# Optimization experiments

Hardware: AMD Instinct MI355X
Metric: run time of the kernel (lower is better)

The kernel has to match this reference:

```python
import jax, jax.numpy as jnp
import numpy as np

B, N, E = 16, 64, 512
C_IMG = 512
H1, H2, H3 = 256, 128, 64
U, R = 8, 8
BBC = 9
EH1, EH2 = 64, 64
BBOX_POS_MAX = 1024.0
EPS = 1e-5


def setup_inputs():
    key = jax.random.key(0)
    ks = jax.random.split(key, 24)
    f = lambda i, shape, s=0.05: jax.random.normal(ks[i], shape, jnp.float32) * s
    return {
        'roi_features': f(0, (B, N, C_IMG), 1.0),
        'batch_bboxes': jax.random.uniform(ks[1], (B, N, 4)) * BBOX_POS_MAX,
        'batch_directions': jax.random.uniform(ks[2], (B, N, 4)),
        'batch_priorities': jax.random.uniform(ks[3], (B, N)),
        'w1': f(4, (C_IMG, H1)), 'b1': f(5, (H1,)),
        'bn1_g': jnp.ones((H1,)), 'bn1_b': jnp.zeros((H1,)),
        'bn1_m': jnp.zeros((H1,)), 'bn1_v': jnp.ones((H1,)),
        'w2': f(6, (H1, H2)), 'b2': f(7, (H2,)),
        'bn2_g': jnp.ones((H2,)), 'bn2_b': jnp.zeros((H2,)),
        'bn2_m': jnp.zeros((H2,)), 'bn2_v': jnp.ones((H2,)),
        'w3': f(8, (H2, H3)), 'b3': f(9, (H3,)),
        'wn': f(10, (H3, U)), 'bn_c': f(11, (U,)),
        'we1': f(12, (2 * BBC, EH1)), 'be1': f(13, (EH1,)),
        'we2': f(14, (EH1, EH2)), 'be2': f(15, (EH2,)),
        'wei': f(16, (EH2, R)), 'bei': f(17, (R,)),
        'edge_index': jax.random.randint(ks[18], (B, 2, E), 0, N, dtype=jnp.int32),
    }


def _bn(x, g, b, m, v):
    # BatchNorm1d in eval mode (running stats)
    return (x - m) * jax.lax.rsqrt(v + EPS) * g + b


def _build_see(edge_index):
    # Padded neighbor table replacing edge_index2dict:
    # see[b,n,0] = n, then srcs of edges with dst==n, in original edge order.
    src = edge_index[:, 0, :]                                   # [B,E]
    dst = edge_index[:, 1, :]                                   # [B,E]
    eq = dst[:, :, None] == dst[:, None, :]                     # [B,E,E]
    lower = jnp.tril(jnp.ones((E, E), bool), -1)
    pos = jnp.sum(eq & lower, axis=-1) + 1                      # rank within dst group, +1 for self slot
    see = jnp.zeros((B, N, N), jnp.int32).at[:, :, 0].set(jnp.arange(N, dtype=jnp.int32))
    b_idx = jnp.arange(B)[:, None]
    see = see.at[b_idx, dst, pos].set(src, mode='drop')
    deg = jnp.zeros((B, N), jnp.int32).at[b_idx, dst].add(1)
    count = jnp.minimum(deg + 1, N)
    mask = (jnp.arange(N)[None, None, :] < count[:, :, None]).astype(jnp.float32)  # [B,N,N]
    return see, mask


def _forward(roi_features, batch_bboxes, batch_directions, batch_priorities,
             w1, b1, bn1_g, bn1_b, bn1_m, bn1_v,
             w2, b2, bn2_g, bn2_b, bn2_m, bn2_v,
             w3, b3, wn, bn_c,
             we1, be1, we2, be2, wei, bei, edge_index):
    see, mask = _build_see(edge_index)
    # --- node branch (node_predictor + node_concept_interpreter) ---
    x = roi_features.reshape(B * N, C_IMG)
    x = jax.nn.relu(_bn(x @ w1 + b1, bn1_g, bn1_b, bn1_m, bn1_v))
    x = jax.nn.relu(_bn(x @ w2 + b2, bn2_g, bn2_b, bn2_m, bn2_v))
    x = jax.nn.relu(x @ w3 + b3)
    node_c = jax.nn.sigmoid(x @ wn + bn_c).reshape(B, N, U)
    # get_nlm_unary_concepts: gather per-node neighborhood into dense [B,N,N,U]
    gu = jax.vmap(lambda u, s: u[s])(node_c, see)               # [B,N,N,U]
    node_concepts = (gu * mask[..., None]).reshape(B * N, N, U)
    # --- edge branch ---
    attr = jnp.concatenate([batch_bboxes / BBOX_POS_MAX, batch_directions,
                            batch_priorities[..., None]], axis=-1)  # [B,N,BBC]
    pair = jnp.concatenate([
        jnp.broadcast_to(attr[:, :, None, :], (B, N, N, BBC)),
        jnp.broadcast_to(attr[:, None, :, :], (B, N, N, BBC))], axis=-1).reshape(-1, 2 * BBC)
    e = jax.nn.relu(pair @ we1 + be1)
    e = jax.nn.relu(e @ we2 + be2)
    rel = jax.nn.sigmoid(e @ wei + bei).reshape(B, N, N, R)
    # get_nlm_binary_concepts: rel[b, see[b,n,i], see[b,n,j]] with zero padding
    def per_b(r, s, m):
        g = r[s[:, :, None], s[:, None, :]]                     # [N,N,N,R]
        return g * (m[:, :, None, None] * m[:, None, :, None])
    edge_concepts = jax.vmap(per_b)(rel, see, mask).reshape(B * N, N, N, R)
    return node_concepts, edge_concepts


def reference(roi_features, batch_bboxes, batch_directions, batch_priorities,
              w1, b1, bn1_g, bn1_b, bn1_m, bn1_v,
              w2, b2, bn2_g, bn2_b, bn2_m, bn2_v,
              w3, b3, wn, bn_c,
              we1, be1, we2, be2, wei, bei, edge_index):
    return _forward(roi_features, batch_bboxes, batch_directions, batch_priorities,
                    w1, b1, bn1_g, bn1_b, bn1_m, bn1_v,
                    w2, b2, bn2_g, bn2_b, bn2_m, bn2_v,
                    w3, b3, wn, bn_c,
                    we1, be1, we2, be2, wei, bei, edge_index)
```

## Files before the change

### kernel.cpp

```cpp
#include <hip/hip_runtime.h>
#include <math.h>

#define BB    16
#define NN    64
#define EE    512
#define CIMG  512
#define H1D   256
#define H2D   128
#define H3D   64
#define UD    8
#define RD    8
#define BBCD  9
#define EH1D  64
#define EH2D  64
#define EPSF  1e-5f

typedef float nfloat4 __attribute__((ext_vector_type(4)));

__global__ __launch_bounds__(256) void fusedA_kernel(
    const int* __restrict__ edge_index,
    const float* __restrict__ bboxes,
    const float* __restrict__ dirs,
    const float* __restrict__ prios,
    const float* __restrict__ we1, const float* __restrict__ be1,
    int* __restrict__ see, int* __restrict__ cnt,
    const float* __restrict__ roi,
    const float* __restrict__ w1, const float* __restrict__ b1,
    const float* __restrict__ g1, const float* __restrict__ bt1,
    const float* __restrict__ m1, const float* __restrict__ v1,
    const float* __restrict__ w2, const float* __restrict__ b2,
    const float* __restrict__ g2, const float* __restrict__ bt2,
    const float* __restrict__ m2, const float* __restrict__ v2,
    const float* __restrict__ w3, const float* __restrict__ b3,
    const float* __restrict__ wn, const float* __restrict__ bnc,
    float* __restrict__ node_c,
    const float* __restrict__ we2, const float* __restrict__ be2,
    const float* __restrict__ wei, const float* __restrict__ bei,
    float* __restrict__ rel)
{
    __shared__ union {
        struct {
            int src[EE];
            int dst[EE];
            int see[NN * NN];
        } p;
        struct {
            float part[4096];
            float h1[4][H1D];
            float h2[4][H2D];
            float h3[4][H3D];
        } n;
        struct {
            float e1[NN * 68];
            float qw[NN * EH1D];
            float wei[EH2D * RD];
            float attr[NN][BBCD];
            float we1[2 * BBCD * EH1D];
            float Pi[EH1D];
            float be2[EH2D];
            float bei[RD];
        } e;
    } sm;

    const int t = threadIdx.x;

    if (blockIdx.x < BB) {
        const int b = blockIdx.x;
        const int* ei = edge_index + b * 2 * EE;
        for (int e = t; e < EE; e += 256) {
            sm.p.src[e] = ei[e];
            sm.p.dst[e] = ei[EE + e];
        }
        for (int x = t; x < NN * NN; x += 256)
            sm.p.see[x] = ((x & (NN - 1)) == 0) ? (x >> 6) : 0;
        __syncthreads();

        if (t < NN) {
            int pos = 0;
            #pragma unroll 8
            for (int e = 0; e < EE; ++e) {
                if (sm.p.dst[e] == t) {
                    ++pos;
                    if (pos < NN) sm.p.see[t * NN + pos] = sm.p.src[e];
                }
            }
            int c = pos + 1;
            cnt[b * NN + t] = (c < NN) ? c : NN;
        }
        __syncthreads();

        int4* dst4 = (int4*)(see + b * NN * NN);
        const int4* src4 = (const int4*)sm.p.see;
        for (int x = t; x < (NN * NN) / 4; x += 256) dst4[x] = src4[x];
        return;
    }

    if (blockIdx.x >= BB + 256) {
        const int id = blockIdx.x - (BB + 256);
        const int b = id >> 6;
        const int i = id & 63;

        if (t < NN) {
            const float* bbp = bboxes + (b * NN + t) * 4;
            const float* ddp = dirs + (b * NN + t) * 4;
            sm.e.attr[t][0] = bbp[0] * (1.0f / 1024.0f);
            sm.e.attr[t][1] = bbp[1] * (1.0f / 1024.0f);
            sm.e.attr[t][2] = bbp[2] * (1.0f / 1024.0f);
            sm.e.attr[t][3] = bbp[3] * (1.0f / 1024.0f);
            sm.e.attr[t][4] = ddp[0];
            sm.e.attr[t][5] = ddp[1];
            sm.e.attr[t][6] = ddp[2];
            sm.e.attr[t][7] = ddp[3];
            sm.e.attr[t][8] = prios[b * NN + t];
        }
        for (int x = t; x < 2 * BBCD * EH1D; x += 256) sm.e.we1[x] = we1[x];
        {
            const float4* w4 = (const float4*)we2;
            float4* qw4 = (float4*)sm.e.qw;
            #pragma unroll
            for (int x = 0; x < 4; ++x) qw4[x * 256 + t] = w4[x * 256 + t];
        }
        if (t < 128) ((float4*)sm.e.wei)[t] = ((const float4*)wei)[t];
        if (t < EH2D) sm.e.be2[t] = be2[t];
        if (t < RD) sm.e.bei[t] = bei[t];
        __syncthreads();

        if (t < EH1D) {
            float p = be1[t];
            #pragma unroll
            for (int c = 0; c < BBCD; ++c)
                p = fmaf(sm.e.attr[i][c], sm.e.we1[c * EH1D + t], p);
            sm.e.Pi[t] = p;
        }
        __syncthreads();

        {
            const int o = t & 63;
            const int jw = t >> 6;
            #pragma unroll
            for (int jg = 0; jg < 16; ++jg) {
                const int j = jg * 4 + jw;
                float a = sm.e.Pi[o];
                #pragma unroll
                for (int c = 0; c < BBCD; ++c)
                    a = fmaf(sm.e.attr[j][c], sm.e.we1[(BBCD + c) * EH1D + o], a);
                sm.e.e1[j * 68 + o] = fmaxf(0.f, a);
            }
        }
        __syncthreads();

        const int tx = t & 15, ty = t >> 4;
        const int o0 = tx * 4, j0 = ty * 4;
        float acc[4][4];
        #pragma unroll
        for (int r = 0; r < 4; ++r)
            #pragma unroll
            for (int o = 0; o < 4; ++o) acc[r][o] = 0.f;

        #pragma unroll 4
        for (int cg = 0; cg < 16; ++cg) {
            float ev[4][4];
            #pragma unroll
            for (int r = 0; r < 4; ++r) {
                float4 v = *(const float4*)(sm.e.e1 + (j0 + r) * 68 + cg * 4);
                ev[r][0] = v.x; ev[r][1] = v.y; ev[r][2] = v.z; ev[r][3] = v.w;
            }
            #pragma unroll
            for (int q = 0; q < 4; ++q) {
                float4 wv = *(const float4*)(sm.e.qw + (cg * 4 + q) * EH1D + o0);
                #pragma unroll
                for (int r = 0; r < 4; ++r) {
                    acc[r][0] = fmaf(ev[r][q], wv.x, acc[r][0]);
                    acc[r][1] = fmaf(ev[r][q], wv.y, acc[r][1]);
                    acc[r][2] = fmaf(ev[r][q], wv.z, acc[r][2]);
                    acc[r][3] = fmaf(ev[r][q], wv.w, acc[r][3]);
                }
            }
        }

        {
            float4 bv = *(const float4*)(sm.e.be2 + o0);
            #pragma unroll
            for (int r = 0; r < 4; ++r) {
                float4 v;
                v.x = fmaxf(0.f, acc[r][0] + bv.x);
                v.y = fmaxf(0.f, acc[r][1] + bv.y);
                v.z = fmaxf(0.f, acc[r][2] + bv.z);
                v.w = fmaxf(0.f, acc[r][3] + bv.w);
                *(float4*)(sm.e.e1 + (j0 + r) * 68 + o0) = v;
            }
        }
        __syncthreads();

        {
            const int j = t >> 2;
            const int r0 = (t & 3) * 2;
            float a0 = sm.e.bei[r0], a1 = sm.e.bei[r0 + 1];
            const float* e2row = sm.e.e1 + j * 68;
            #pragma unroll
            for (int og = 0; og < 16; ++og) {
                float4 e2v = *(const float4*)(e2row + og * 4);
                float2 w0 = *(const float2*)(sm.e.wei + (og * 4 + 0) * RD + r0);
                float2 w1 = *(const float2*)(sm.e.wei + (og * 4 + 1) * RD + r0);
                float2 w2 = *(const float2*)(sm.e.wei + (og * 4 + 2) * RD + r0);
                float2 w3 = *(const float2*)(sm.e.wei + (og * 4 + 3) * RD + r0);
                a0 = fmaf(e2v.x, w0.x, a0); a1 = fmaf(e2v.x, w0.y, a1);
                a0 = fmaf(e2v.y, w1.x, a0); a1 = fmaf(e2v.y, w1.y, a1);
                a0 = fmaf(e2v.z, w2.x, a0); a1 = fmaf(e2v.z, w2.y, a1);
                a0 = fmaf(e2v.w, w3.x, a0); a1 = fmaf(e2v.w, w3.y, a1);
            }
            float2 o;
            o.x = 1.f / (1.f + expf(-a0));
            o.y = 1.f / (1.f + expf(-a1));
            *(float2*)(rel + ((size_t)id * NN + j) * RD + r0) = o;
        }
        return;
    }

    const int row0 = (blockIdx.x - BB) * 4;
    float* part = sm.n.part;

    {
        const int og = t & 63, kg = t >> 6;
        const float4* w1v = (const float4*)w1;
        const float4* roiv = (const float4*)(roi + (size_t)row0 * CIMG);
        float acc[4][4];
        #pragma unroll
        for (int r = 0; r < 4; ++r)
            #pragma unroll
            for (int c = 0; c < 4; ++c) acc[r][c] = 0.f;

        for (int cq = 0; cq < 32; ++cq) {
            const int c4 = kg * 32 + cq;
            float x[4][4], w[4][4];
            #pragma unroll
            for (int r = 0; r < 4; ++r) {
                float4 v = roiv[r * 128 + c4];
                x[r][0] = v.x; x[r][1] = v.y; x[r][2] = v.z; x[r][3] = v.w;
            }
            #pragma unroll
            for (int q = 0; q < 4; ++q) {
                float4 v = w1v[(size_t)(c4 * 4 + q) * 64 + og];
                w[q][0] = v.x; w[q][1] = v.y; w[q][2] = v.z; w[q][3] = v.w;
            }
            #pragma unroll
            for (int r = 0; r < 4; ++r)
                #pragma unroll
                for (int q = 0; q < 4; ++q)
                    #pragma unroll
                    for (int c = 0; c < 4; ++c)
                        acc[r][c] = fmaf(x[r][q], w[q][c], acc[r][c]);
        }
        #pragma unroll
        for (int r = 0; r < 4; ++r) {
            float4 v = {acc[r][0], acc[r][1], acc[r][2], acc[r][3]};
            *(float4*)(part + (kg * 4 + r) * 256 + og * 4) = v;
        }
    }
    __syncthreads();
    {
        const int o = t;
        const float bias = b1[o];
        const float scale = rsqrtf(v1[o] + EPSF) * g1[o];
        const float beta = bt1[o];
        const float mu = m1[o];
        #pragma unroll
        for (int r = 0; r < 4; ++r) {
            float s = part[(0 * 4 + r) * 256 + o] + part[(1 * 4 + r) * 256 + o]
                    + part[(2 * 4 + r) * 256 + o] + part[(3 * 4 + r) * 256 + o];
            sm.n.h1[r][o] = fmaxf(0.f, (s + bias - mu) * scale + beta);
        }
    }
    __syncthreads();

    {
        const int og = t & 31, kg = t >> 5;
        const float4* w2v = (const float4*)w2;
        float acc[4][4];
        #pragma unroll
        for (int r = 0; r < 4; ++r)
            #pragma unroll
            for (int c = 0; c < 4; ++c) acc[r][c] = 0.f;

        #pragma unroll
        for (int cq = 0; cq < 8; ++cq) {
            const int c4 = kg * 8 + cq;
            float x[4][4], w[4][4];
            #pragma unroll
            for (int r = 0; r < 4; ++r) {
                float4 v = *(const float4*)&sm.n.h1[r][c4 * 4];
                x[r][0] = v.x; x[r][1] = v.y; x[r][2] = v.z; x[r][3] = v.w;
            }
            #pragma unroll
            for (int q = 0; q < 4; ++q) {
                float4 v = w2v[(size_t)(c4 * 4 + q) * 32 + og];
                w[q][0] = v.x; w[q][1] = v.y; w[q][2] = v.z; w[q][3] = v.w;
            }
            #pragma unroll
            for (int r = 0; r < 4; ++r)
                #pragma unroll
                for (int q = 0; q < 4; ++q)
                    #pragma unroll
                    for (int c = 0; c < 4; ++c)
                        acc[r][c] = fmaf(x[r][q], w[q][c], acc[r][c]);
        }
        #pragma unroll
        for (int r = 0; r < 4; ++r) {
            float4 v = {acc[r][0], acc[r][1], acc[r][2], acc[r][3]};
            *(float4*)(part + (kg * 4 + r) * 128 + og * 4) = v;
        }
    }
    __syncthreads();
    {
        const int o = t & 127;
        const int rp = t >> 7;
        const float bias = b2[o];
        const float scale = rsqrtf(v2[o] + EPSF) * g2[o];
        const float beta = bt2[o];
        const float mu = m2[o];
        #pragma unroll
        for (int rr = 0; rr < 2; ++rr) {
            const int r = rp + rr * 2;
            float s = 0.f;
            #pragma unroll
            for (int kg = 0; kg < 8; ++kg) s += part[(kg * 4 + r) * 128 + o];
            sm.n.h2[r][o] = fmaxf(0.f, (s + bias - mu) * scale + beta);
        }
    }
    __syncthreads();

    {
        const int og = t & 15, kg = t >> 4;
        const float4* w3v = (const float4*)w3;
        float acc[4][4];
        #pragma unroll
        for (int r = 0; r < 4; ++r)
            #pragma unroll
            for (int c = 0; c < 4; ++c) acc[r][c] = 0.f;

        #pragma unroll
        for (int cq = 0; cq < 2; ++cq) {
            const int c4 = kg * 2 + cq;
            float x[4][4], w[4][4];
            #pragma unroll
            for (int r = 0; r < 4; ++r) {
                float4 v = *(const float4*)&sm.n.h2[r][c4 * 4];
                x[r][0] = v.x; x[r][1] = v.y; x[r][2] = v.z; x[r][3] = v.w;
            }
            #pragma unroll
            for (int q = 0; q < 4; ++q) {
                float4 v = w3v[(size_t)(c4 * 4 + q) * 16 + og];
                w[q][0] = v.x; w[q][1] = v.y; w[q][2] = v.z; w[q][3] = v.w;
            }
            #pragma unroll
            for (int r = 0; r < 4; ++r)
                #pragma unroll
                for (int q = 0; q < 4; ++q)
                    #pragma unroll
                    for (int c = 0; c < 4; ++c)
                        acc[r][c] = fmaf(x[r][q], w[q][c], acc[r][c]);
        }
        #pragma unroll
        for (int r = 0; r < 4; ++r) {
            float4 v = {acc[r][0], acc[r][1], acc[r][2], acc[r][3]};
            *(float4*)(part + (kg * 4 + r) * 64 + og * 4) = v;
        }
    }
    __syncthreads();
    {
        const int o = t & 63;
        const int r = t >> 6;
        float s = b3[o];
        #pragma unroll
        for (int kg = 0; kg < 16; ++kg) s += part[(kg * 4 + r) * 64 + o];
        sm.n.h3[r][o] = fmaxf(0.f, s);
    }
    __syncthreads();

    if (t < 32) {
        const int o = t & 7, r = t >> 3;
        float a = bnc[o];
        #pragma unroll 8
        for (int c = 0; c < H3D; ++c) a = fmaf(sm.n.h3[r][c], wn[c * UD + o], a);
        node_c[(size_t)(row0 + r) * UD + o] = 1.f / (1.f + expf(-a));
    }
}

__global__ __launch_bounds__(256) void gatherfill_kernel(
    const int* __restrict__ see, const int* __restrict__ cnt,
    const float* __restrict__ node_c, const float* __restrict__ rel,
    float* __restrict__ out_node, float* __restrict__ out_edge)
{
    __shared__ int s_s[NN];

    const int t = threadIdx.x;
    const int bi = blockIdx.x;
    const int b = bi >> 6;
    const int c = cnt[bi];

    if (t < NN) s_s[t] = see[bi * NN + t];
    __syncthreads();

    if (t < NN) {
        const float m = (t < c) ? 1.f : 0.f;
        const float4* src = (const float4*)(node_c + (size_t)(b * NN + s_s[t]) * UD);
        float4 v0 = src[0], v1 = src[1];
        v0.x *= m; v0.y *= m; v0.z *= m; v0.w *= m;
        v1.x *= m; v1.y *= m; v1.z *= m; v1.w *= m;
        float4* dst = (float4*)(out_node + ((size_t)bi * NN + t) * UD);
        dst[0] = v0;
        dst[1] = v1;
    }

    const float* relb = rel + (size_t)b * NN * NN * RD;
    float* outb = out_edge + (size_t)bi * NN * NN * RD;
    const nfloat4 z = {0.f, 0.f, 0.f, 0.f};

    #pragma unroll
    for (int it = 0; it < (NN * NN) / 256; ++it) {
        const int task = it * 256 + t;
        const int j = task >> 6;
        const int k = task & 63;
        nfloat4* dst = (nfloat4*)(outb + (size_t)task * RD);
        if (j < c) {
            if (k < c) {
                const float4* src =
                    (const float4*)(relb + (size_t)(s_s[j] * NN + s_s[k]) * RD);
                float4 v0 = src[0], v1 = src[1];
                ((float4*)dst)[0] = v0;
                ((float4*)dst)[1] = v1;
            } else {
                __builtin_nontemporal_store(z, dst);
                __builtin_nontemporal_store(z, dst + 1);
            }
        } else {
            __builtin_nontemporal_store(z, dst);
            __builtin_nontemporal_store(z, dst + 1);
        }
    }
}

extern "C" void kernel_launch(void* const* d_in, const int* in_sizes, int n_in,
                              void* d_out, int out_size, void* d_ws, size_t ws_size,
                              hipStream_t stream)
{
    const float* roi  = (const float*)d_in[0];
    const float* bbox = (const float*)d_in[1];
    const float* dirs = (const float*)d_in[2];
    const float* prio = (const float*)d_in[3];
    const float* w1   = (const float*)d_in[4];
    const float* b1   = (const float*)d_in[5];
    const float* g1   = (const float*)d_in[6];
    const float* bt1  = (const float*)d_in[7];
    const float* m1   = (const float*)d_in[8];
    const float* v1   = (const float*)d_in[9];
    const float* w2   = (const float*)d_in[10];
    const float* b2   = (const float*)d_in[11];
    const float* g2   = (const float*)d_in[12];
    const float* bt2  = (const float*)d_in[13];
    const float* m2   = (const float*)d_in[14];
    const float* v2   = (const float*)d_in[15];
    const float* w3   = (const float*)d_in[16];
    const float* b3   = (const float*)d_in[17];
    const float* wn   = (const float*)d_in[18];
    const float* bnc  = (const float*)d_in[19];
    const float* we1  = (const float*)d_in[20];
    const float* be1  = (const float*)d_in[21];
    const float* we2  = (const float*)d_in[22];
    const float* be2  = (const float*)d_in[23];
    const float* wei  = (const float*)d_in[24];
    const float* bei  = (const float*)d_in[25];
    const int* edge_index = (const int*)d_in[26];

    char* ws = (char*)d_ws;
    int*   see    = (int*)ws;   ws += (size_t)BB * NN * NN * 4;
    int*   cnt    = (int*)ws;   ws += (size_t)BB * NN * 4;
    float* node_c = (float*)ws; ws += (size_t)BB * NN * UD * 4;
    float* rel    = (float*)ws; ws += (size_t)BB * NN * NN * RD * 4;

    float* out_node = (float*)d_out;
    float* out_edge = (float*)d_out + (size_t)BB * NN * NN * UD;

    hipLaunchKernelGGL(fusedA_kernel,
                       dim3(BB + 256 + BB * NN), dim3(256), 0, stream,
                       edge_index, bbox, dirs, prio, we1, be1,
                       see, cnt,
                       roi, w1, b1, g1, bt1, m1, v1,
                       w2, b2, g2, bt2, m2, v2,
                       w3, b3, wn, bnc, node_c,
                       we2, be2, wei, bei, rel);
    hipLaunchKernelGGL(gatherfill_kernel, dim3(BB * NN), dim3(256), 0, stream,
                       see, cnt, node_c, rel, out_node, out_edge);
}
```

Before: 246.6 us.

## Move edge output zero-fill into first kernel and copy only valid corner

Adds extra blocks to the fused first kernel that zero the entire edge-concept output with nontemporal stores, so the fill overlaps with node and edge MLP compute. The second kernel now writes only the valid c-by-c corner gathered from rel, with no branching per element. Separately, the row mapping in the edge MLP tile is changed to interleave rows, to alter the LDS access pattern. Corner elements are written twice, which relies on ordering across kernels on the same stream.

```diff
diff --git a/kernel.cpp b/kernel.cpp
--- a/kernel.cpp
+++ b/kernel.cpp
@@ -16,6 +16,12 @@
 #define EPSF  1e-5f
 
 typedef float nfloat4 __attribute__((ext_vector_type(4)));
+
+#define GRID_PREP  BB
+#define GRID_NODE  256
+#define GRID_EDGE  (BB * NN)
+#define GRID_FILL  2048
+#define FILL_BASE  (GRID_PREP + GRID_NODE + GRID_EDGE)
 
 __global__ __launch_bounds__(256) void fusedA_kernel(
     const int* __restrict__ edge_index,
@@ -36,8 +42,21 @@
     float* __restrict__ node_c,
     const float* __restrict__ we2, const float* __restrict__ be2,
     const float* __restrict__ wei, const float* __restrict__ bei,
-    float* __restrict__ rel)
+    float* __restrict__ rel,
+    float* __restrict__ out_edge)
 {
+    const int t = threadIdx.x;
+
+    if (blockIdx.x >= FILL_BASE) {
+        const int f = blockIdx.x - FILL_BASE;
+        const nfloat4 z = {0.f, 0.f, 0.f, 0.f};
+        float* base = out_edge + (size_t)f * 16384 + t * 4;
+        #pragma unroll
+        for (int i = 0; i < 16; ++i)
+            __builtin_nontemporal_store(z, (nfloat4*)(base + i * 1024));
+        return;
+    }
+
     __shared__ union {
         struct {
             int src[EE];
@@ -62,8 +81,6 @@
         } e;
     } sm;
 
-    const int t = threadIdx.x;
-
     if (blockIdx.x < BB) {
         const int b = blockIdx.x;
         const int* ei = edge_index + b * 2 * EE;
@@ -95,8 +112,8 @@
         return;
     }
 
-    if (blockIdx.x >= BB + 256) {
-        const int id = blockIdx.x - (BB + 256);
+    if (blockIdx.x >= BB + GRID_NODE) {
+        const int id = blockIdx.x - (BB + GRID_NODE);
         const int b = id >> 6;
         const int i = id & 63;
 
@@ -150,7 +167,7 @@
         __syncthreads();
 
         const int tx = t & 15, ty = t >> 4;
-        const int o0 = tx * 4, j0 = ty * 4;
+        const int o0 = tx * 4;
         float acc[4][4];
         #pragma unroll
         for (int r = 0; r < 4; ++r)
@@ -162,7 +179,7 @@
             float ev[4][4];
             #pragma unroll
             for (int r = 0; r < 4; ++r) {
-                float4 v = *(const float4*)(sm.e.e1 + (j0 + r) * 68 + cg * 4);
+                float4 v = *(const float4*)(sm.e.e1 + (ty + 16 * r) * 68 + cg * 4);
                 ev[r][0] = v.x; ev[r][1] = v.y; ev[r][2] = v.z; ev[r][3] = v.w;
             }
             #pragma unroll
@@ -187,7 +204,7 @@
                 v.y = fmaxf(0.f, acc[r][1] + bv.y);
                 v.z = fmaxf(0.f, acc[r][2] + bv.z);
                 v.w = fmaxf(0.f, acc[r][3] + bv.w);
-                *(float4*)(sm.e.e1 + (j0 + r) * 68 + o0) = v;
+                *(float4*)(sm.e.e1 + (ty + 16 * r) * 68 + o0) = v;
             }
         }
         __syncthreads();
@@ -386,7 +403,7 @@
     }
 }
 
-__global__ __launch_bounds__(256) void gatherfill_kernel(
+__global__ __launch_bounds__(256) void corner_kernel(
     const int* __restrict__ see, const int* __restrict__ cnt,
     const float* __restrict__ node_c, const float* __restrict__ rel,
     float* __restrict__ out_node, float* __restrict__ out_edge)
@@ -414,28 +431,18 @@
 
     const float* relb = rel + (size_t)b * NN * NN * RD;
     float* outb = out_edge + (size_t)bi * NN * NN * RD;
-    const nfloat4 z = {0.f, 0.f, 0.f, 0.f};
-
-    #pragma unroll
-    for (int it = 0; it < (NN * NN) / 256; ++it) {
-        const int task = it * 256 + t;
-        const int j = task >> 6;
-        const int k = task & 63;
-        nfloat4* dst = (nfloat4*)(outb + (size_t)task * RD);
-        if (j < c) {
-            if (k < c) {
-                const float4* src =
-                    (const float4*)(relb + (size_t)(s_s[j] * NN + s_s[k]) * RD);
-                float4 v0 = src[0], v1 = src[1];
-                ((float4*)dst)[0] = v0;
-                ((float4*)dst)[1] = v1;
-            } else {
-                __builtin_nontemporal_store(z, dst);
-                __builtin_nontemporal_store(z, dst + 1);
-            }
-        } else {
-            __builtin_nontemporal_store(z, dst);
-            __builtin_nontemporal_store(z, dst + 1);
+
+    const int w = t >> 6;
+    const int k = t & 63;
+    if (k < c) {
+        const int sk = s_s[k];
+        for (int j = w; j < c; j += 4) {
+            const float4* src =
+                (const float4*)(relb + (size_t)(s_s[j] * NN + sk) * RD);
+            float4 v0 = src[0], v1 = src[1];
+            float4* dst = (float4*)(outb + (size_t)(j * NN + k) * RD);
+            dst[0] = v0;
+            dst[1] = v1;
         }
     }
 }
@@ -482,13 +489,14 @@
     float* out_edge = (float*)d_out + (size_t)BB * NN * NN * UD;
 
     hipLaunchKernelGGL(fusedA_kernel,
-                       dim3(BB + 256 + BB * NN), dim3(256), 0, stream,
+                       dim3(FILL_BASE + GRID_FILL), dim3(256), 0, stream,
                        edge_index, bbox, dirs, prio, we1, be1,
                        see, cnt,
                        roi, w1, b1, g1, bt1, m1, v1,
                        w2, b2, g2, bt2, m2, v2,
                        w3, b3, wn, bnc, node_c,
-                       we2, be2, wei, bei, rel);
-    hipLaunchKernelGGL(gatherfill_kernel, dim3(BB * NN), dim3(256), 0, stream,
+                       we2, be2, wei, bei, rel,
+                       out_edge);
+    hipLaunchKernelGGL(corner_kernel, dim3(BB * NN), dim3(256), 0, stream,
                        see, cnt, node_c, rel, out_node, out_edge);
 }
```

New measurement: 234.7 us. 1.05x faster.

## Recompute edge MLP per output slab and drop rel workspace gather

Applied to the files above, without the earlier changes.

The edge MLP no longer runs once per (b,i) row into a global rel buffer that a second kernel gathers from. The edge-slab kernel now evaluates the MLP only for the c×c valid (j,k) pairs of each slab, using precomputed per-neighbor P/Q projections, and writes sigmoid outputs straight into the output. Padded regions get nontemporal zero stores. This removes the rel workspace write and its gathered re-read, at the cost of duplicated MLP work across slabs that share a batch and an extra per-tile synchronization loop.

```diff
diff --git a/kernel.cpp b/kernel.cpp
--- a/kernel.cpp
+++ b/kernel.cpp
@@ -17,12 +17,9 @@
 
 typedef float nfloat4 __attribute__((ext_vector_type(4)));
 
-__global__ __launch_bounds__(256) void fusedA_kernel(
+
+__global__ __launch_bounds__(256) void prepnode_kernel(
     const int* __restrict__ edge_index,
-    const float* __restrict__ bboxes,
-    const float* __restrict__ dirs,
-    const float* __restrict__ prios,
-    const float* __restrict__ we1, const float* __restrict__ be1,
     int* __restrict__ see, int* __restrict__ cnt,
     const float* __restrict__ roi,
     const float* __restrict__ w1, const float* __restrict__ b1,
@@ -33,10 +30,7 @@
     const float* __restrict__ m2, const float* __restrict__ v2,
     const float* __restrict__ w3, const float* __restrict__ b3,
     const float* __restrict__ wn, const float* __restrict__ bnc,
-    float* __restrict__ node_c,
-    const float* __restrict__ we2, const float* __restrict__ be2,
-    const float* __restrict__ wei, const float* __restrict__ bei,
-    float* __restrict__ rel)
+    float* __restrict__ node_c)
 {
     __shared__ union {
         struct {
@@ -50,16 +44,6 @@
             float h2[4][H2D];
             float h3[4][H3D];
         } n;
-        struct {
-            float e1[NN * 68];
-            float qw[NN * EH1D];
-            float wei[EH2D * RD];
-            float attr[NN][BBCD];
-            float we1[2 * BBCD * EH1D];
-            float Pi[EH1D];
-            float be2[EH2D];
-            float bei[RD];
-        } e;
     } sm;
 
     const int t = threadIdx.x;
@@ -95,91 +79,334 @@
         return;
     }
 
-    if (blockIdx.x >= BB + 256) {
-        const int id = blockIdx.x - (BB + 256);
-        const int b = id >> 6;
-        const int i = id & 63;
-
-        if (t < NN) {
-            const float* bbp = bboxes + (b * NN + t) * 4;
-            const float* ddp = dirs + (b * NN + t) * 4;
-            sm.e.attr[t][0] = bbp[0] * (1.0f / 1024.0f);
-            sm.e.attr[t][1] = bbp[1] * (1.0f / 1024.0f);
-            sm.e.attr[t][2] = bbp[2] * (1.0f / 1024.0f);
-            sm.e.attr[t][3] = bbp[3] * (1.0f / 1024.0f);
-            sm.e.attr[t][4] = ddp[0];
-            sm.e.attr[t][5] = ddp[1];
-            sm.e.attr[t][6] = ddp[2];
-            sm.e.attr[t][7] = ddp[3];
-            sm.e.attr[t][8] = prios[b * NN + t];
-        }
-        for (int x = t; x < 2 * BBCD * EH1D; x += 256) sm.e.we1[x] = we1[x];
+    const int row0 = (blockIdx.x - BB) * 4;
+    float* part = sm.n.part;
+
+    {
+        const int og = t & 63, kg = t >> 6;
+        const float4* w1v = (const float4*)w1;
+        const float4* roiv = (const float4*)(roi + (size_t)row0 * CIMG);
+        float acc[4][4];
+        #pragma unroll
+        for (int r = 0; r < 4; ++r)
+            #pragma unroll
+            for (int c = 0; c < 4; ++c) acc[r][c] = 0.f;
+
+        for (int cq = 0; cq < 32; ++cq) {
+            const int c4 = kg * 32 + cq;
+            float x[4][4], w[4][4];
+            #pragma unroll
+            for (int r = 0; r < 4; ++r) {
+                float4 v = roiv[r * 128 + c4];
+                x[r][0] = v.x; x[r][1] = v.y; x[r][2] = v.z; x[r][3] = v.w;
+            }
+            #pragma unroll
+            for (int q = 0; q < 4; ++q) {
+                float4 v = w1v[(size_t)(c4 * 4 + q) * 64 + og];
+                w[q][0] = v.x; w[q][1] = v.y; w[q][2] = v.z; w[q][3] = v.w;
+            }
+            #pragma unroll
+            for (int r = 0; r < 4; ++r)
+                #pragma unroll
+                for (int q = 0; q < 4; ++q)
+                    #pragma unroll
+                    for (int c = 0; c < 4; ++c)
+                        acc[r][c] = fmaf(x[r][q], w[q][c], acc[r][c]);
+        }
+        #pragma unroll
+        for (int r = 0; r < 4; ++r) {
+            float4 v = {acc[r][0], acc[r][1], acc[r][2], acc[r][3]};
+            *(float4*)(part + (kg * 4 + r) * 256 + og * 4) = v;
+        }
+    }
+    __syncthreads();
+    {
+        const int o = t;
+        const float bias = b1[o];
+        const float scale = rsqrtf(v1[o] + EPSF) * g1[o];
+        const float beta = bt1[o];
+        const float mu = m1[o];
+        #pragma unroll
+        for (int r = 0; r < 4; ++r) {
+            float s = part[(0 * 4 + r) * 256 + o] + part[(1 * 4 + r) * 256 + o]
+                    + part[(2 * 4 + r) * 256 + o] + part[(3 * 4 + r) * 256 + o];
+            sm.n.h1[r][o] = fmaxf(0.f, (s + bias - mu) * scale + beta);
+        }
+    }
+    __syncthreads();
+
+    {
+        const int og = t & 31, kg = t >> 5;
+        const float4* w2v = (const float4*)w2;
+        float acc[4][4];
+        #pragma unroll
+        for (int r = 0; r < 4; ++r)
+            #pragma unroll
+            for (int c = 0; c < 4; ++c) acc[r][c] = 0.f;
+
+        #pragma unroll
+        for (int cq = 0; cq < 8; ++cq) {
+            const int c4 = kg * 8 + cq;
+            float x[4][4], w[4][4];
+            #pragma unroll
+            for (int r = 0; r < 4; ++r) {
+                float4 v = *(const float4*)&sm.n.h1[r][c4 * 4];
+                x[r][0] = v.x; x[r][1] = v.y; x[r][2] = v.z; x[r][3] = v.w;
+            }
+            #pragma unroll
+            for (int q = 0; q < 4; ++q) {
+                float4 v = w2v[(size_t)(c4 * 4 + q) * 32 + og];
+                w[q][0] = v.x; w[q][1] = v.y; w[q][2] = v.z; w[q][3] = v.w;
+            }
+            #pragma unroll
+            for (int r = 0; r < 4; ++r)
+                #pragma unroll
+                for (int q = 0; q < 4; ++q)
+                    #pragma unroll
+                    for (int c = 0; c < 4; ++c)
+                        acc[r][c] = fmaf(x[r][q], w[q][c], acc[r][c]);
+        }
+        #pragma unroll
+        for (int r = 0; r < 4; ++r) {
+            float4 v = {acc[r][0], acc[r][1], acc[r][2], acc[r][3]};
+            *(float4*)(part + (kg * 4 + r) * 128 + og * 4) = v;
+        }
+    }
+    __syncthreads();
+    {
+        const int o = t & 127;
+        const int rp = t >> 7;
+        const float bias = b2[o];
+        const float scale = rsqrtf(v2[o] + EPSF) * g2[o];
+        const float beta = bt2[o];
+        const float mu = m2[o];
+        #pragma unroll
+        for (int rr = 0; rr < 2; ++rr) {
+            const int r = rp + rr * 2;
+            float s = 0.f;
+            #pragma unroll
+            for (int kg = 0; kg < 8; ++kg) s += part[(kg * 4 + r) * 128 + o];
+            sm.n.h2[r][o] = fmaxf(0.f, (s + bias - mu) * scale + beta);
+        }
+    }
+    __syncthreads();
+
+    {
+        const int og = t & 15, kg = t >> 4;
+        const float4* w3v = (const float4*)w3;
+        float acc[4][4];
+        #pragma unroll
+        for (int r = 0; r < 4; ++r)
+            #pragma unroll
+            for (int c = 0; c < 4; ++c) acc[r][c] = 0.f;
+
+        #pragma unroll
+        for (int cq = 0; cq < 2; ++cq) {
+            const int c4 = kg * 2 + cq;
+            float x[4][4], w[4][4];
+            #pragma unroll
+            for (int r = 0; r < 4; ++r) {
+                float4 v = *(const float4*)&sm.n.h2[r][c4 * 4];
+                x[r][0] = v.x; x[r][1] = v.y; x[r][2] = v.z; x[r][3] = v.w;
+            }
+            #pragma unroll
+            for (int q = 0; q < 4; ++q) {
+                float4 v = w3v[(size_t)(c4 * 4 + q) * 16 + og];
+                w[q][0] = v.x; w[q][1] = v.y; w[q][2] = v.z; w[q][3] = v.w;
+            }
+            #pragma unroll
+            for (int r = 0; r < 4; ++r)
+                #pragma unroll
+                for (int q = 0; q < 4; ++q)
+                    #pragma unroll
+                    for (int c = 0; c < 4; ++c)
+                        acc[r][c] = fmaf(x[r][q], w[q][c], acc[r][c]);
+        }
+        #pragma unroll
+        for (int r = 0; r < 4; ++r) {
+            float4 v = {acc[r][0], acc[r][1], acc[r][2], acc[r][3]};
+            *(float4*)(part + (kg * 4 + r) * 64 + og * 4) = v;
+        }
+    }
+    __syncthreads();
+    {
+        const int o = t & 63;
+        const int r = t >> 6;
+        float s = b3[o];
+        #pragma unroll
+        for (int kg = 0; kg < 16; ++kg) s += part[(kg * 4 + r) * 64 + o];
+        sm.n.h3[r][o] = fmaxf(0.f, s);
+    }
+    __syncthreads();
+
+    if (t < 32) {
+        const int o = t & 7, r = t >> 3;
+        float a = bnc[o];
+        #pragma unroll 8
+        for (int c = 0; c < H3D; ++c) a = fmaf(sm.n.h3[r][c], wn[c * UD + o], a);
+        node_c[(size_t)(row0 + r) * UD + o] = 1.f / (1.f + expf(-a));
+    }
+}
+
+__global__ __launch_bounds__(256) void edgeslab_kernel(
+    const float* __restrict__ bboxes,
+    const float* __restrict__ dirs,
+    const float* __restrict__ prios,
+    const float* __restrict__ we1, const float* __restrict__ be1,
+    const float* __restrict__ we2, const float* __restrict__ be2,
+    const float* __restrict__ wei, const float* __restrict__ bei,
+    const int* __restrict__ see, const int* __restrict__ cnt,
+    const float* __restrict__ node_c,
+    float* __restrict__ out_node, float* __restrict__ out_edge)
+{
+    __shared__ float e1L[NN * 68];
+    __shared__ float PL[NN * NN];
+    __shared__ float QL[NN * NN];
+    __shared__ float qwL[NN * EH1D];
+    __shared__ float attrL[NN][BBCD];
+    __shared__ float we1L[2 * BBCD * EH1D];
+    __shared__ float weiL[EH2D * RD];
+    __shared__ float be1L[EH1D];
+    __shared__ float be2L[EH2D];
+    __shared__ float beiL[RD];
+    __shared__ int   sLi[NN];
+    __shared__ int   jkL[64];
+
+    const int t = threadIdx.x;
+    const int bi = blockIdx.x;
+    const int b = bi >> 6;
+    const int c = cnt[bi];
+
+    if (t < NN) sLi[t] = see[bi * NN + t];
+    if (t < NN) {
+        const float* bbp = bboxes + (b * NN + t) * 4;
+        const float* ddp = dirs + (b * NN + t) * 4;
+        attrL[t][0] = bbp[0] * (1.0f / 1024.0f);
+        attrL[t][1] = bbp[1] * (1.0f / 1024.0f);
+        attrL[t][2] = bbp[2] * (1.0f / 1024.0f);
+        attrL[t][3] = bbp[3] * (1.0f / 1024.0f);
+        attrL[t][4] = ddp[0];
+        attrL[t][5] = ddp[1];
+        attrL[t][6] = ddp[2];
+        attrL[t][7] = ddp[3];
+        attrL[t][8] = prios[b * NN + t];
+    }
+    for (int x = t; x < 2 * BBCD * EH1D; x += 256) we1L[x] = we1[x];
+    {
+        const float4* w4 = (const float4*)we2;
+        float4* qw4 = (float4*)qwL;
+        #pragma unroll
+        for (int x = 0; x < 4; ++x) qw4[x * 256 + t] = w4[x * 256 + t];
+    }
+    if (t < 128) ((float4*)weiL)[t] = ((const float4*)wei)[t];
+    if (t < EH1D) be1L[t] = be1[t];
+    if (t < EH2D) be2L[t] = be2[t];
+    if (t < RD)   beiL[t] = bei[t];
+    __syncthreads();
+
+    if (t < NN) {
+        const float m = (t < c) ? 1.f : 0.f;
+        const float4* src = (const float4*)(node_c + (size_t)(b * NN + sLi[t]) * UD);
+        float4 v0 = src[0], v1 = src[1];
+        v0.x *= m; v0.y *= m; v0.z *= m; v0.w *= m;
+        v1.x *= m; v1.y *= m; v1.z *= m; v1.w *= m;
+        float4* dst = (float4*)(out_node + ((size_t)bi * NN + t) * UD);
+        dst[0] = v0;
+        dst[1] = v1;
+    }
+
+    {
+        const int o = t & 63, jw = t >> 6;
+        #pragma unroll
+        for (int jg = 0; jg < 16; ++jg) {
+            const int j = jg * 4 + jw;
+            const int n = sLi[j];
+            float p = be1L[o], q = 0.f;
+            #pragma unroll
+            for (int cc = 0; cc < BBCD; ++cc) {
+                p = fmaf(attrL[n][cc], we1L[cc * EH1D + o], p);
+                q = fmaf(attrL[n][cc], we1L[(BBCD + cc) * EH1D + o], q);
+            }
+            PL[j * NN + o] = p;
+            QL[j * NN + o] = q;
+        }
+    }
+
+    float* slab = out_edge + (size_t)bi * (NN * NN * RD);
+    {
+        const nfloat4 z = {0.f, 0.f, 0.f, 0.f};
+        const int nrow4 = (NN - c) * 128;
+        for (int x = t; x < nrow4; x += 256) {
+            const int row = c + (x >> 7);
+            __builtin_nontemporal_store(
+                z, (nfloat4*)(slab + (size_t)row * 512 + (size_t)(x & 127) * 4));
+        }
+        const int w = NN - c;
+        const int ntail = c * w * 2;
+        for (int x = t; x < ntail; x += 256) {
+            const int e = x >> 1, h = x & 1;
+            const int j = e / w;
+            const int k = c + (e - j * w);
+            __builtin_nontemporal_store(
+                z, (nfloat4*)(slab + (size_t)(j * NN + k) * RD + h * 4));
+        }
+    }
+    __syncthreads();
+
+    const int npairs = c * c;
+    const int ntiles = (npairs + 63) >> 6;
+    for (int tt = 0; tt < ntiles; ++tt) {
+        const int base = tt << 6;
+        if (t < 64) {
+            const int p = base + t;
+            int u = 0xFFFF;
+            if (p < npairs) { const int j = p / c; u = (j << 8) | (p - j * c); }
+            jkL[t] = u;
+        }
+        __syncthreads();
+
         {
-            const float4* w4 = (const float4*)we2;
-            float4* qw4 = (float4*)sm.e.qw;
-            #pragma unroll
-            for (int x = 0; x < 4; ++x) qw4[x * 256 + t] = w4[x * 256 + t];
-        }
-        if (t < 128) ((float4*)sm.e.wei)[t] = ((const float4*)wei)[t];
-        if (t < EH2D) sm.e.be2[t] = be2[t];
-        if (t < RD) sm.e.bei[t] = bei[t];
+            const int o = t & 63, pw = t >> 6;
+            #pragma unroll
+            for (int pg = 0; pg < 16; ++pg) {
+                const int row = pg * 4 + pw;
+                const int u = jkL[row];
+                const int jj = (u >> 8) & 63, kk = u & 63;
+                e1L[row * 68 + o] = fmaxf(0.f, PL[jj * NN + o] + QL[kk * NN + o]);
+            }
+        }
         __syncthreads();
 
-        if (t < EH1D) {
-            float p = be1[t];
-            #pragma unroll
-            for (int c = 0; c < BBCD; ++c)
-                p = fmaf(sm.e.attr[i][c], sm.e.we1[c * EH1D + t], p);
-            sm.e.Pi[t] = p;
-        }
-        __syncthreads();
-
         {
-            const int o = t & 63;
-            const int jw = t >> 6;
-            #pragma unroll
-            for (int jg = 0; jg < 16; ++jg) {
-                const int j = jg * 4 + jw;
-                float a = sm.e.Pi[o];
+            const int tx = t & 15, ty = t >> 4;
+            const int o0 = tx * 4;
+            float acc[4][4];
+            #pragma unroll
+            for (int r = 0; r < 4; ++r)
                 #pragma unroll
-                for (int c = 0; c < BBCD; ++c)
-                    a = fmaf(sm.e.attr[j][c], sm.e.we1[(BBCD + c) * EH1D + o], a);
-                sm.e.e1[j * 68 + o] = fmaxf(0.f, a);
-            }
-        }
-        __syncthreads();
-
-        const int tx = t & 15, ty = t >> 4;
-        const int o0 = tx * 4, j0 = ty * 4;
-        float acc[4][4];
-        #pragma unroll
-        for (int r = 0; r < 4; ++r)
-            #pragma unroll
-            for (int o = 0; o < 4; ++o) acc[r][o] = 0.f;
-
-        #pragma unroll 4
-        for (int cg = 0; cg < 16; ++cg) {
-            float ev[4][4];
-            #pragma unroll
-            for (int r = 0; r < 4; ++r) {
-                float4 v = *(const float4*)(sm.e.e1 + (j0 + r) * 68 + cg * 4);
-                ev[r][0] = v.x; ev[r][1] = v.y; ev[r][2] = v.z; ev[r][3] = v.w;
-            }
-            #pragma unroll
-            for (int q = 0; q < 4; ++q) {
-                float4 wv = *(const float4*)(sm.e.qw + (cg * 4 + q) * EH1D + o0);
+                for (int o = 0; o < 4; ++o) acc[r][o] = 0.f;
+
+            #pragma unroll 4
+            for (int cg = 0; cg < 16; ++cg) {
+                float ev[4][4];
                 #pragma unroll
                 for (int r = 0; r < 4; ++r) {
-                    acc[r][0] = fmaf(ev[r][q], wv.x, acc[r][0]);
-                    acc[r][1] = fmaf(ev[r][q], wv.y, acc[r][1]);
-                    acc[r][2] = fmaf(ev[r][q], wv.z, acc[r][2]);
-                    acc[r][3] = fmaf(ev[r][q], wv.w, acc[r][3]);
+                    float4 v = *(const float4*)(e1L + (ty + 16 * r) * 68 + cg * 4);
+                    ev[r][0] = v.x; ev[r][1] = v.y; ev[r][2] = v.z; ev[r][3] = v.w;
                 }
-            }
-        }
-
-        {
-            float4 bv = *(const float4*)(sm.e.be2 + o0);
+                #pragma unroll
+                for (int q = 0; q < 4; ++q) {
+                    float4 wv = *(const float4*)(qwL + (cg * 4 + q) * EH1D + o0);
+                    #pragma unroll
+                    for (int r = 0; r < 4; ++r) {
+                        acc[r][0] = fmaf(ev[r][q], wv.x, acc[r][0]);
+                        acc[r][1] = fmaf(ev[r][q], wv.y, acc[r][1]);
+                        acc[r][2] = fmaf(ev[r][q], wv.z, acc[r][2]);
+                        acc[r][3] = fmaf(ev[r][q], wv.w, acc[r][3]);
+                    }
+                }
+            }
+            float4 bv = *(const float4*)(be2L + o0);
             #pragma unroll
             for (int r = 0; r < 4; ++r) {
                 float4 v;
@@ -187,256 +414,38 @@
                 v.y = fmaxf(0.f, acc[r][1] + bv.y);
                 v.z = fmaxf(0.f, acc[r][2] + bv.z);
                 v.w = fmaxf(0.f, acc[r][3] + bv.w);
-                *(float4*)(sm.e.e1 + (j0 + r) * 68 + o0) = v;
+                *(float4*)(e1L + (ty + 16 * r) * 68 + o0) = v;
             }
         }
         __syncthreads();
 
         {
-            const int j = t >> 2;
+            const int row = t >> 2;
             const int r0 = (t & 3) * 2;
-            float a0 = sm.e.bei[r0], a1 = sm.e.bei[r0 + 1];
-            const float* e2row = sm.e.e1 + j * 68;
+            const int u = jkL[row];
+            float a0 = beiL[r0], a1 = beiL[r0 + 1];
+            const float* e2row = e1L + row * 68;
             #pragma unroll
             for (int og = 0; og < 16; ++og) {
                 float4 e2v = *(const float4*)(e2row + og * 4);
-                float2 w0 = *(const float2*)(sm.e.wei + (og * 4 + 0) * RD + r0);
-                float2 w1 = *(const float2*)(sm.e.wei + (og * 4 + 1) * RD + r0);
-                float2 w2 = *(const float2*)(sm.e.wei + (og * 4 + 2) * RD + r0);
-                float2 w3 = *(const float2*)(sm.e.wei + (og * 4 + 3) * RD + r0);
+                float2 w0 = *(const float2*)(weiL + (og * 4 + 0) * RD + r0);
+                float2 w1 = *(const float2*)(weiL + (og * 4 + 1) * RD + r0);
+                float2 w2 = *(const float2*)(weiL + (og * 4 + 2) * RD + r0);
+                float2 w3 = *(const float2*)(weiL + (og * 4 + 3) * RD + r0);
                 a0 = fmaf(e2v.x, w0.x, a0); a1 = fmaf(e2v.x, w0.y, a1);
                 a0 = fmaf(e2v.y, w1.x, a0); a1 = fmaf(e2v.y, w1.y, a1);
                 a0 = fmaf(e2v.z, w2.x, a0); a1 = fmaf(e2v.z, w2.y, a1);
                 a0 = fmaf(e2v.w, w3.x, a0); a1 = fmaf(e2v.w, w3.y, a1);
             }
-            float2 o;
-            o.x = 1.f / (1.f + expf(-a0));
-            o.y = 1.f / (1.f + expf(-a1));
-            *(float2*)(rel + ((size_t)id * NN + j) * RD + r0) = o;
-        }
-        return;
-    }
-
-    const int row0 = (blockIdx.x - BB) * 4;
-    float* part = sm.n.part;
-
-    {
-        const int og = t & 63, kg = t >> 6;
-        const float4* w1v = (const float4*)w1;
-        const float4* roiv = (const float4*)(roi + (size_t)row0 * CIMG);
-        float acc[4][4];
-        #pragma unroll
-        for (int r = 0; r < 4; ++r)
-            #pragma unroll
-            for (int c = 0; c < 4; ++c) acc[r][c] = 0.f;
-
-        for (int cq = 0; cq < 32; ++cq) {
-            const int c4 = kg * 32 + cq;
-            float x[4][4], w[4][4];
-            #pragma unroll
-            for (int r = 0; r < 4; ++r) {
-                float4 v = roiv[r * 128 + c4];
-                x[r][0] = v.x; x[r][1] = v.y; x[r][2] = v.z; x[r][3] = v.w;
-            }
-            #pragma unroll
-            for (int q = 0; q < 4; ++q) {
-                float4 v = w1v[(size_t)(c4 * 4 + q) * 64 + og];
-                w[q][0] = v.x; w[q][1] = v.y; w[q][2] = v.z; w[q][3] = v.w;
-            }
-            #pragma unroll
-            for (int r = 0; r < 4; ++r)
-                #pragma unroll
-                for (int q = 0; q < 4; ++q)
-                    #pragma unroll
-                    for (int c = 0; c < 4; ++c)
-                        acc[r][c] = fmaf(x[r][q], w[q][c], acc[r][c]);
-        }
-        #pragma unroll
-        for (int r = 0; r < 4; ++r) {
-            float4 v = {acc[r][0], acc[r][1], acc[r][2], acc[r][3]};
-            *(float4*)(part + (kg * 4 + r) * 256 + og * 4) = v;
-        }
-    }
-    __syncthreads();
-    {
-        const int o = t;
-        const float bias = b1[o];
-        const float scale = rsqrtf(v1[o] + EPSF) * g1[o];
-        const float beta = bt1[o];
-        const float mu = m1[o];
-        #pragma unroll
-        for (int r = 0; r < 4; ++r) {
-            float s = part[(0 * 4 + r) * 256 + o] + part[(1 * 4 + r) * 256 + o]
-                    + part[(2 * 4 + r) * 256 + o] + part[(3 * 4 + r) * 256 + o];
-            sm.n.h1[r][o] = fmaxf(0.f, (s + bias - mu) * scale + beta);
-        }
-    }
-    __syncthreads();
-
-    {
-        const int og = t & 31, kg = t >> 5;
-        const float4* w2v = (const float4*)w2;
-        float acc[4][4];
-        #pragma unroll
-        for (int r = 0; r < 4; ++r)
-            #pragma unroll
-            for (int c = 0; c < 4; ++c) acc[r][c] = 0.f;
-
-        #pragma unroll
-        for (int cq = 0; cq < 8; ++cq) {
-            const int c4 = kg * 8 + cq;
-            float x[4][4], w[4][4];
-            #pragma unroll
-            for (int r = 0; r < 4; ++r) {
-                float4 v = *(const float4*)&sm.n.h1[r][c4 * 4];
-                x[r][0] = v.x; x[r][1] = v.y; x[r][2] = v.z; x[r][3] = v.w;
-            }
-            #pragma unroll
-            for (int q = 0; q < 4; ++q) {
-                float4 v = w2v[(size_t)(c4 * 4 + q) * 32 + og];
-                w[q][0] = v.x; w[q][1] = v.y; w[q][2] = v.z; w[q][3] = v.w;
-            }
-            #pragma unroll
-            for (int r = 0; r < 4; ++r)
-                #pragma unroll
-                for (int q = 0; q < 4; ++q)
-                    #pragma unroll
-                    for (int c = 0; c < 4; ++c)
-                        acc[r][c] = fmaf(x[r][q], w[q][c], acc[r][c]);
-        }
-        #pragma unroll
-        for (int r = 0; r < 4; ++r) {
-            float4 v = {acc[r][0], acc[r][1], acc[r][2], acc[r][3]};
-            *(float4*)(part + (kg * 4 + r) * 128 + og * 4) = v;
-        }
-    }
-    __syncthreads();
-    {
-        const int o = t & 127;
-        const int rp = t >> 7;
-        const float bias = b2[o];
-        const float scale = rsqrtf(v2[o] + EPSF) * g2[o];
-        const float beta = bt2[o];
-        const float mu = m2[o];
-        #pragma unroll
-        for (int rr = 0; rr < 2; ++rr) {
-            const int r = rp + rr * 2;
-            float s = 0.f;
-            #pragma unroll
-            for (int kg = 0; kg < 8; ++kg) s += part[(kg * 4 + r) * 128 + o];
-            sm.n.h2[r][o] = fmaxf(0.f, (s + bias - mu) * scale + beta);
-        }
-    }
-    __syncthreads();
-
-    {
-        const int og = t & 15, kg = t >> 4;
-        const float4* w3v = (const float4*)w3;
-        float acc[4][4];
-        #pragma unroll
-        for (int r = 0; r < 4; ++r)
-            #pragma unroll
-            for (int c = 0; c < 4; ++c) acc[r][c] = 0.f;
-
-        #pragma unroll
-        for (int cq = 0; cq < 2; ++cq) {
-            const int c4 = kg * 2 + cq;
-            float x[4][4], w[4][4];
-            #pragma unroll
-            for (int r = 0; r < 4; ++r) {
-                float4 v = *(const float4*)&sm.n.h2[r][c4 * 4];
-                x[r][0] = v.x; x[r][1] = v.y; x[r][2] = v.z; x[r][3] = v.w;
-            }
-            #pragma unroll
-            for (int q = 0; q < 4; ++q) {
-                float4 v = w3v[(size_t)(c4 * 4 + q) * 16 + og];
-                w[q][0] = v.x; w[q][1] = v.y; w[q][2] = v.z; w[q][3] = v.w;
-            }
-            #pragma unroll
-            for (int r = 0; r < 4; ++r)
-                #pragma unroll
-                for (int q = 0; q < 4; ++q)
-                    #pragma unroll
-                    for (int c = 0; c < 4; ++c)
-                        acc[r][c] = fmaf(x[r][q], w[q][c], acc[r][c]);
-        }
-        #pragma unroll
-        for (int r = 0; r < 4; ++r) {
-            float4 v = {acc[r][0], acc[r][1], acc[r][2], acc[r][3]};
-            *(float4*)(part + (kg * 4 + r) * 64 + og * 4) = v;
-        }
-    }
-    __syncthreads();
-    {
-        const int o = t & 63;
-        const int r = t >> 6;
-        float s = b3[o];
-        #pragma unroll
-        for (int kg = 0; kg < 16; ++kg) s += part[(kg * 4 + r) * 64 + o];
-        sm.n.h3[r][o] = fmaxf(0.f, s);
-    }
-    __syncthreads();
-
-    if (t < 32) {
-        const int o = t & 7, r = t >> 3;
-        float a = bnc[o];
-        #pragma unroll 8
-        for (int c = 0; c < H3D; ++c) a = fmaf(sm.n.h3[r][c], wn[c * UD + o], a);
-        node_c[(size_t)(row0 + r) * UD + o] = 1.f / (1.f + expf(-a));
-    }
-}
-
-__global__ __launch_bounds__(256) void gatherfill_kernel(
-    const int* __restrict__ see, const int* __restrict__ cnt,
-    const float* __restrict__ node_c, const float* __restrict__ rel,
-    float* __restrict__ out_node, float* __restrict__ out_edge)
-{
-    __shared__ int s_s[NN];
-
-    const int t = threadIdx.x;
-    const int bi = blockIdx.x;
-    const int b = bi >> 6;
-    const int c = cnt[bi];
-
-    if (t < NN) s_s[t] = see[bi * NN + t];
-    __syncthreads();
-
-    if (t < NN) {
-        const float m = (t < c) ? 1.f : 0.f;
-        const float4* src = (const float4*)(node_c + (size_t)(b * NN + s_s[t]) * UD);
-        float4 v0 = src[0], v1 = src[1];
-        v0.x *= m; v0.y *= m; v0.z *= m; v0.w *= m;
-        v1.x *= m; v1.y *= m; v1.z *= m; v1.w *= m;
-        float4* dst = (float4*)(out_node + ((size_t)bi * NN + t) * UD);
-        dst[0] = v0;
-        dst[1] = v1;
-    }
-
-    const float* relb = rel + (size_t)b * NN * NN * RD;
-    float* outb = out_edge + (size_t)bi * NN * NN * RD;
-    const nfloat4 z = {0.f, 0.f, 0.f, 0.f};
-
-    #pragma unroll
-    for (int it = 0; it < (NN * NN) / 256; ++it) {
-        const int task = it * 256 + t;
-        const int j = task >> 6;
-        const int k = task & 63;
-        nfloat4* dst = (nfloat4*)(outb + (size_t)task * RD);
-        if (j < c) {
-            if (k < c) {
-                const float4* src =
-                    (const float4*)(relb + (size_t)(s_s[j] * NN + s_s[k]) * RD);
-                float4 v0 = src[0], v1 = src[1];
-                ((float4*)dst)[0] = v0;
-                ((float4*)dst)[1] = v1;
-            } else {
-                __builtin_nontemporal_store(z, dst);
-                __builtin_nontemporal_store(z, dst + 1);
-            }
-        } else {
-            __builtin_nontemporal_store(z, dst);
-            __builtin_nontemporal_store(z, dst + 1);
-        }
+            if (u != 0xFFFF) {
+                const int j = u >> 8, k = u & 255;
+                float2 o2;
+                o2.x = 1.f / (1.f + expf(-a0));
+                o2.y = 1.f / (1.f + expf(-a1));
+                *(float2*)(slab + (size_t)(j * NN + k) * RD + r0) = o2;
+            }
+        }
+        __syncthreads();
     }
 }
 
@@ -476,19 +485,17 @@
     int*   see    = (int*)ws;   ws += (size_t)BB * NN * NN * 4;
     int*   cnt    = (int*)ws;   ws += (size_t)BB * NN * 4;
     float* node_c = (float*)ws; ws += (size_t)BB * NN * UD * 4;
-    float* rel    = (float*)ws; ws += (size_t)BB * NN * NN * RD * 4;
 
     float* out_node = (float*)d_out;
     float* out_edge = (float*)d_out + (size_t)BB * NN * NN * UD;
 
-    hipLaunchKernelGGL(fusedA_kernel,
-                       dim3(BB + 256 + BB * NN), dim3(256), 0, stream,
-                       edge_index, bbox, dirs, prio, we1, be1,
-                       see, cnt,
+    hipLaunchKernelGGL(prepnode_kernel,
+                       dim3(BB + 256), dim3(256), 0, stream,
+                       edge_index, see, cnt,
                        roi, w1, b1, g1, bt1, m1, v1,
                        w2, b2, g2, bt2, m2, v2,
-                       w3, b3, wn, bnc, node_c,
-                       we2, be2, wei, bei, rel);
-    hipLaunchKernelGGL(gatherfill_kernel, dim3(BB * NN), dim3(256), 0, stream,
-                       see, cnt, node_c, rel, out_node, out_edge);
+                       w3, b3, wn, bnc, node_c);
+    hipLaunchKernelGGL(edgeslab_kernel, dim3(BB * NN), dim3(256), 0, stream,
+                       bbox, dirs, prio, we1, be1, we2, be2, wei, bei,
+                       see, cnt, node_c, out_node, out_edge);
 }
```

New measurement: 283.1 us. 14.8% more time.
